# Performance work log

Measured on AMD Instinct MI355X. Metric: run time of the kernel, lower is better.

The kernel has to match this reference:

```python
import jax, jax.numpy as jnp
import numpy as np

B, S, D, H = 16, 512, 1024, 4096
TOP_K = H // 4  # default: hidden_dim // 4


def setup_inputs() -> dict:
    key = jax.random.key(0)
    ks = jax.random.split(key, 11)
    s = lambda fan_in: 1.0 / np.sqrt(fan_in)
    return {
        "inputs": jax.random.normal(ks[0], (B, S, D), jnp.float32),
        "up_w": jax.random.uniform(ks[1], (H, D), jnp.float32, -s(D), s(D)),
        "up_b": jax.random.uniform(ks[2], (H,), jnp.float32, -s(D), s(D)),
        "gate_w1": jax.random.uniform(ks[3], (H, D), jnp.float32, -s(D), s(D)),
        "gate_b1": jax.random.uniform(ks[4], (H,), jnp.float32, -s(D), s(D)),
        "gate_w2": jax.random.uniform(ks[5], (H, H), jnp.float32, -s(H), s(H)),
        "gate_b2": jax.random.uniform(ks[6], (H,), jnp.float32, -s(H), s(H)),
        "mod_w": jax.random.uniform(ks[7], (H, D), jnp.float32, -s(D), s(D)),
        "mod_b": jax.random.uniform(ks[8], (H,), jnp.float32, -s(D), s(D)),
        "down_w": jax.random.uniform(ks[9], (D, H), jnp.float32, -s(H), s(H)),
        "down_b": jax.random.uniform(ks[10], (D,), jnp.float32, -s(H), s(H)),
    }


def reference(inputs, up_w, up_b, gate_w1, gate_b1, gate_w2, gate_b2,
              mod_w, mod_b, down_w, down_b):
    b, s_len, d = inputs.shape
    h_dim = up_w.shape[0]
    # gate MLP -> scores [B, S, H]
    scores = jax.nn.relu(jnp.einsum('bsd,hd->bsh', inputs, gate_w1) + gate_b1)
    scores = jnp.einsum('bsh,gh->bsg', scores, gate_w2) + gate_b2
    flat = scores.reshape(b, s_len * h_dim)
    k = min(TOP_K * s_len, s_len * h_dim)
    _, flat_idx = jax.lax.top_k(flat, k)                    # [B, k]
    hidden_idx = flat_idx % h_dim                           # [B, k]
    # mask[b, h] = True if row h of up.weight was overwritten by mod.weight
    # (duplicate indices write the same value, so set-semantics are exact)
    mask = jnp.zeros((b, h_dim), bool).at[
        jnp.arange(b)[:, None], hidden_idx].set(True)       # [B, H]
    # Instead of materializing per-batch [B,H,D] weights, compute both shared-
    # weight GEMMs and select per (batch, hidden) row — identical math.
    h_up = jnp.einsum('bsd,hd->bsh', inputs, up_w) + up_b
    h_mod = jnp.einsum('bsd,hd->bsh', inputs, mod_w) + mod_b
    h = jnp.where(mask[:, None, :], h_mod, h_up)            # [B, S, H]
    h = jax.nn.silu(h)
    # dropout is identity in eval/reference mode
    return jnp.einsum('bsh,dh->bsd', h, down_w) + down_b
```

## Files before the change

kernel.cpp:

```cpp
#include <hip/hip_runtime.h>
#include <cstdint>

typedef __attribute__((ext_vector_type(4))) _Float16 f16x4;
typedef __attribute__((ext_vector_type(8))) _Float16 f16x8;
typedef __attribute__((ext_vector_type(4))) float f32x4;

#define D_DIM 1024
#define H_DIM 4096
#define BS_ROWS 8192
#define K_SEL 524288u
#define CAND_CAP 32768u

__device__ __forceinline__ unsigned lkey(float v){
  float u = fmaf(v, 67108864.f, 268435456.f);
  u = fminf(fmaxf(u, 0.f), 536870911.f);
  return (unsigned)u;
}

__device__ __forceinline__ void gload16(const _Float16* g, _Float16* l){
  __builtin_amdgcn_global_load_lds(
      (const __attribute__((address_space(1))) void*)g,
      (__attribute__((address_space(3))) void*)l, 16, 0, 0);
}

template<int N> __device__ __forceinline__ void waitcnt_vm(){
  if      constexpr (N == 0) asm volatile("s_waitcnt vmcnt(0)" ::: "memory");
  else if constexpr (N == 4) asm volatile("s_waitcnt vmcnt(4)" ::: "memory");
  else if constexpr (N == 6) asm volatile("s_waitcnt vmcnt(6)" ::: "memory");
  else                       asm volatile("s_waitcnt vmcnt(8)" ::: "memory");
}

__device__ __forceinline__ size_t img_g32(int row, int k8, int nkt32){
  int p = (row & 127) >> 1;
  int s = (((row & 1) << 2) | (k8 & 3)) ^ (p & 7);
  return ((size_t)((row >> 7) * nkt32 + (k8 >> 2)) << 9) + (p << 3) + s;
}

__global__ __launch_bounds__(256)
void pack_all(const float* __restrict__ X, const float* __restrict__ g1w,
              const float* __restrict__ g2w, const float* __restrict__ upw,
              const float* __restrict__ modw, const float* __restrict__ dww,
              _Float16* __restrict__ Xhi, _Float16* __restrict__ Xlo,
              _Float16* __restrict__ G1hi, _Float16* __restrict__ G1lo,
              _Float16* __restrict__ G2hi, _Float16* __restrict__ G2lo,
              _Float16* __restrict__ UPhi, _Float16* __restrict__ MODhi,
              _Float16* __restrict__ DWhi)
{
  unsigned g = blockIdx.x * 256u + threadIdx.x;
  const float* W; _Float16* hi; _Float16* lo = nullptr;
  int k8s, n32; unsigned base;
  if      (g < 1048576u){ W=X;    hi=Xhi;  lo=Xlo;  k8s=7; n32=32;  base=0u;        }
  else if (g < 1572864u){ W=g1w;  hi=G1hi; lo=G1lo; k8s=7; n32=32;  base=1048576u; }
  else if (g < 3670016u){ W=g2w;  hi=G2hi; lo=G2lo; k8s=9; n32=128; base=1572864u; }
  else if (g < 4194304u){ W=upw;  hi=UPhi;          k8s=7; n32=32;  base=3670016u; }
  else if (g < 4718592u){ W=modw; hi=MODhi;         k8s=7; n32=32;  base=4194304u; }
  else                  { W=dww;  hi=DWhi;          k8s=9; n32=128; base=4718592u; }
  g -= base;
  int row = (int)(g >> k8s), k8 = (int)(g & ((1u << k8s) - 1u));
  const float* src = W + ((size_t)row << (k8s + 3)) + (k8 << 3);
  float4 f0 = *(const float4*)src, f1 = *(const float4*)(src + 4);
  float ff[8] = {f0.x,f0.y,f0.z,f0.w,f1.x,f1.y,f1.z,f1.w};
  f16x8 hv, lv;
  #pragma unroll
  for (int i = 0; i < 8; i++){
    hv[i] = (_Float16)ff[i];
    lv[i] = (_Float16)(ff[i] - (float)hv[i]);
  }
  size_t d = img_g32(row, k8, n32) << 3;
  *(f16x8*)&hi[d] = hv;
  if (lo) *(f16x8*)&lo[d] = lv;
}

enum { MODE_G1 = 0, MODE_G2 = 1, MODE_UPMOD = 2, MODE_DOWN = 3 };

template<int MODE>
__global__ __launch_bounds__(256)
void gemm_t(const _Float16* __restrict__ Ahi, const _Float16* __restrict__ Alo,
            const _Float16* __restrict__ Bhi, const _Float16* __restrict__ Blo,
            const float* __restrict__ bias0, const float* __restrict__ bias1,
            const unsigned* __restrict__ mask,
            _Float16* __restrict__ Chi, _Float16* __restrict__ Clo,
            float* __restrict__ C32,
            int N, int K, int m_img_base, int c_row_base)
{
  constexpr int NSEG = (MODE == MODE_G1) ? 3 : 1;
  constexpr bool BSEL = (MODE == MODE_UPMOD);
  constexpr int NLD = (NSEG == 3) ? 8 : 4;
  constexpr int DEPTH = (NSEG == 3) ? 2 : 3;
  __shared__ __align__(16) _Float16 sA [DEPTH][4096];
  __shared__ __align__(16) _Float16 sB [DEPTH][4096];
  __shared__ __align__(16) _Float16 sAl[NSEG == 3 ? 2 : 1][NSEG == 3 ? 4096 : 8];
  __shared__ __align__(16) _Float16 sBl[NSEG == 3 ? 2 : 1][NSEG == 3 ? 4096 : 8];

  const int nbx = gridDim.x;
  const int h = blockIdx.y * nbx + blockIdx.x;
  const int xcd = h & 7, idx = h >> 3;
  const int cw = nbx >> 2;
  const int ch = gridDim.y >> 1;
  const int bx = (xcd & 3) * cw + idx % cw;
  const int by = (xcd >> 2) * ch + idx / cw;

  const int tid = threadIdx.x;
  const int lane = tid & 63;
  const int w  = tid >> 6;
  const int wr = w >> 1, wc = w & 1;
  const int lr = lane & 15;
  const int q  = lane >> 4;

  const int m0 = m_img_base + by * 128;
  const int n0 = bx * 128;
  const int nkt = K >> 5;
  const size_t arow = (size_t)(m0 >> 7) * nkt;
  const size_t brow = (size_t)(n0 >> 7) * nkt;

  const _Float16* bsrcl[2];
  if (BSEL){
    const int bb = m0 >> 9;
    #pragma unroll
    for (int j = 0; j < 2; j++){
      int gi = (w*2 + j)*64 + lane;
      int p = gi >> 3, x = (gi & 7) ^ (p & 7);
      int row = (p << 1) | (x >> 2);
      bsrcl[j] = (mask[bb * H_DIM + n0 + row] ? Blo : Bhi) + (gi << 3);
    }
    waitcnt_vm<0>();
  }

  f32x4 acc[4][4];
  #pragma unroll
  for (int i = 0; i < 4; i++)
    #pragma unroll
    for (int j = 0; j < 4; j++) acc[i][j] = (f32x4){0.f,0.f,0.f,0.f};

  const int soff = (((((lr & 1) << 2) | q) ^ (lr >> 1)) << 3);

  auto STAGE = [&](int buf, int kt){
    const _Float16* at = Ahi + ((arow + kt) << 12);
    #pragma unroll
    for (int j = 0; j < 2; j++)
      gload16(at + ((w*2 + j) << 9) + (lane << 3), &sA[buf][(w*2 + j) << 9]);
    if (NSEG == 3){
      const _Float16* alt = Alo + ((arow + kt) << 12);
      const _Float16* bht = Bhi + ((brow + kt) << 12);
      const _Float16* blt = Blo + ((brow + kt) << 12);
      #pragma unroll
      for (int j = 0; j < 2; j++){
        gload16(alt + ((w*2 + j) << 9) + (lane << 3), &sAl[buf][(w*2 + j) << 9]);
        gload16(bht + ((w*2 + j) << 9) + (lane << 3), &sB [buf][(w*2 + j) << 9]);
        gload16(blt + ((w*2 + j) << 9) + (lane << 3), &sBl[buf][(w*2 + j) << 9]);
      }
    } else if (BSEL){
      const size_t toff = (brow + kt) << 12;
      #pragma unroll
      for (int j = 0; j < 2; j++)
        gload16(bsrcl[j] + toff, &sB[buf][(w*2 + j) << 9]);
    } else {
      const _Float16* bht = Bhi + ((brow + kt) << 12);
      #pragma unroll
      for (int j = 0; j < 2; j++)
        gload16(bht + ((w*2 + j) << 9) + (lane << 3), &sB[buf][(w*2 + j) << 9]);
    }
  };

  STAGE(0, 0);
  if (DEPTH == 3) STAGE(1, 1);

  for (int kt = 0; kt < nkt; ++kt){
    const int rem = nkt - 1 - kt;
    const int cur = (DEPTH == 2) ? (kt & 1) : (kt % 3);
    if (DEPTH == 2){
      if (rem >= 1){ STAGE((kt + 1) & 1, kt + 1); waitcnt_vm<NLD>(); }
      else         { waitcnt_vm<0>(); }
    } else {
      if (rem >= 2){ STAGE((kt + 2) % 3, kt + 2); waitcnt_vm<8>(); }
      else if (rem == 1){ waitcnt_vm<4>(); }
      else         { waitcnt_vm<0>(); }
    }
    __builtin_amdgcn_s_barrier();
    __builtin_amdgcn_sched_barrier(0);

    f16x8 fah[4], fbh[4], fal[4], fbl[4];
    #pragma unroll
    for (int i = 0; i < 4; i++){
      const int ap = ((wr*32 + i*8 + (lr >> 1)) << 6) + soff;
      const int bp = ((wc*32 + i*8 + (lr >> 1)) << 6) + soff;
      fah[i] = *(const f16x8*)&sA[cur][ap];
      fbh[i] = *(const f16x8*)&sB[cur][bp];
      if (NSEG == 3){
        fal[i] = *(const f16x8*)&sAl[cur][ap];
        fbl[i] = *(const f16x8*)&sBl[cur][bp];
      }
    }
    #pragma unroll
    for (int mi = 0; mi < 4; mi++)
      #pragma unroll
      for (int ni = 0; ni < 4; ni++)
        acc[mi][ni] = __builtin_amdgcn_mfma_f32_16x16x32_f16(fah[mi], fbh[ni], acc[mi][ni], 0,0,0);
    if (NSEG == 3){
      #pragma unroll
      for (int mi = 0; mi < 4; mi++)
        #pragma unroll
        for (int ni = 0; ni < 4; ni++)
          acc[mi][ni] = __builtin_amdgcn_mfma_f32_16x16x32_f16(fal[mi], fbh[ni], acc[mi][ni], 0,0,0);
      #pragma unroll
      for (int mi = 0; mi < 4; mi++)
        #pragma unroll
        for (int ni = 0; ni < 4; ni++)
          acc[mi][ni] = __builtin_amdgcn_mfma_f32_16x16x32_f16(fah[mi], fbl[ni], acc[mi][ni], 0,0,0);
    }
    __builtin_amdgcn_s_barrier();
  }

  #pragma unroll
  for (int ni = 0; ni < 4; ni++){
    const int gc = n0 + wc*64 + ni*16 + lr;
    float bias;
    if (MODE == MODE_UPMOD) bias = mask[(m0 >> 9) * H_DIM + gc] ? bias1[gc] : bias0[gc];
    else                    bias = bias0[gc];
    #pragma unroll
    for (int mi = 0; mi < 4; mi++){
      #pragma unroll
      for (int r = 0; r < 4; r++){
        const int gr = m0 + wr*64 + mi*16 + q*4 + r;
        const int cr = gr - c_row_base;
        float v = acc[mi][ni][r] + bias;
        if (MODE == MODE_G1){
          v = fmaxf(v, 0.f);
          size_t d = (img_g32(cr, gc >> 3, N >> 5) << 3) + (gc & 7);
          Chi[d] = (_Float16)v;
        }
        if (MODE == MODE_UPMOD){
          v = v / (1.f + __expf(-v));
          size_t d = (img_g32(cr, gc >> 3, N >> 5) << 3) + (gc & 7);
          Chi[d] = (_Float16)v;
        }
        if (MODE == MODE_DOWN) C32[(size_t)cr * N + gc] = v;
      }
    }
  }
}

__global__ __launch_bounds__(512, 2)
void gemm_g2(const _Float16* __restrict__ A, const _Float16* __restrict__ B,
             const float* __restrict__ bias0,
             unsigned* __restrict__ keys, unsigned* __restrict__ Mkey,
             unsigned* __restrict__ hist, int N, int K, int batch_base)
{
  __shared__ __align__(16) _Float16 sAb[3][8192];
  __shared__ __align__(16) _Float16 sBb[3][8192];

  const int nbx = gridDim.x;
  const int h = blockIdx.y * nbx + blockIdx.x;
  const int xcd = h & 7, idx = h >> 3;
  const int cw = nbx >> 2, ch = gridDim.y >> 1;
  const int bx = (xcd & 3) * cw + idx % cw;
  const int by = (xcd >> 2) * ch + idx / cw;

  const int tid = threadIdx.x;
  const int lane = tid & 63;
  const int w = tid >> 6;
  const int wrow = w >> 2, wcol = w & 3;
  const int lr = lane & 15;
  const int q = lane >> 4;

  const int m0 = by * 256;
  const int n0 = bx * 256;
  const int nkt = K >> 5;
  const int ar0 = (m0 >> 7) * nkt;
  const int br0 = (n0 >> 7) * nkt;

  f32x4 acc[8][4];
  #pragma unroll
  for (int i = 0; i < 8; i++)
    #pragma unroll
    for (int j = 0; j < 4; j++) acc[i][j] = (f32x4){0.f,0.f,0.f,0.f};

  const int soff = (((((lr & 1) << 2) | q) ^ (lr >> 1)) << 3);
  int offA[8], offB[4];
  #pragma unroll
  for (int mi = 0; mi < 8; mi++) offA[mi] = ((mi*8 + (lr >> 1)) << 6) + soff;
  #pragma unroll
  for (int ni = 0; ni < 4; ni++)
    offB[ni] = (((wcol & 1)*32 + ni*8 + (lr >> 1)) << 6) + soff;
  const int arb = wrow * 4096;
  const int bcb = (wcol >> 1) * 4096;

  auto STA = [&](int buf, int rb, int kt){
    gload16(A + ((((size_t)(ar0 + rb*nkt + kt) << 9) + tid) << 3),
            &sAb[buf][rb*4096 + (tid << 3)]);
  };
  auto STB = [&](int buf, int cb, int kt){
    gload16(B + ((((size_t)(br0 + cb*nkt + kt) << 9) + tid) << 3),
            &sBb[buf][cb*4096 + (tid << 3)]);
  };

#define G2PHASE(P, STG)                                                        \
  {                                                                            \
    f16x8 a0 = *(const f16x8*)&sAb[cur][arb + offA[2*(P)]];                    \
    f16x8 a1 = *(const f16x8*)&sAb[cur][arb + offA[2*(P)+1]];                  \
    STG;                                                                       \
    if ((P) == 3){ if (pf) waitcnt_vm<4>(); else waitcnt_vm<0>(); }            \
    __builtin_amdgcn_s_barrier();                                              \
    asm volatile("s_waitcnt lgkmcnt(0)" ::: "memory");                         \
    __builtin_amdgcn_sched_barrier(0);                                         \
    __builtin_amdgcn_s_setprio(1);                                             \
    _Pragma("unroll")                                                          \
    for (int ni = 0; ni < 4; ni++)                                             \
      acc[2*(P)][ni]   = __builtin_amdgcn_mfma_f32_16x16x32_f16(a0, fb[ni], acc[2*(P)][ni], 0,0,0);   \
    _Pragma("unroll")                                                          \
    for (int ni = 0; ni < 4; ni++)                                             \
      acc[2*(P)+1][ni] = __builtin_amdgcn_mfma_f32_16x16x32_f16(a1, fb[ni], acc[2*(P)+1][ni], 0,0,0); \
    __builtin_amdgcn_s_setprio(0);                                             \
    __builtin_amdgcn_s_barrier();                                              \
  }

  STA(0,0,0); STB(0,0,0); STB(0,1,0); STA(0,1,0);
  STA(1,0,1); STB(1,0,1); STB(1,1,1); STA(1,1,1);
  waitcnt_vm<4>();
  __builtin_amdgcn_s_barrier();

  for (int kt = 0; kt < nkt; ++kt){
    const int cur = kt % 3, nb = (kt + 2) % 3;
    const bool pf = (kt + 2 < nkt);
    f16x8 fb[4];
    #pragma unroll
    for (int ni = 0; ni < 4; ni++)
      fb[ni] = *(const f16x8*)&sBb[cur][bcb + offB[ni]];
    G2PHASE(0, if (pf) STA(nb, 0, kt+2))
    G2PHASE(1, if (pf) STB(nb, 0, kt+2))
    G2PHASE(2, if (pf) STB(nb, 1, kt+2))
    G2PHASE(3, if (pf) STA(nb, 1, kt+2))
  }
#undef G2PHASE

  unsigned* lh = (unsigned*)&sAb[0][0];
  __syncthreads();
  for (int i = tid; i < 4096; i += 512) lh[i] = 0;
  __syncthreads();

  const int gb = batch_base + (m0 >> 9);
  #pragma unroll
  for (int ni = 0; ni < 4; ni++){
    const int gc = n0 + wcol*64 + ni*16 + lr;
    const float bias = bias0[gc];
    unsigned colmax = 0u;
    #pragma unroll
    for (int mi = 0; mi < 8; mi++){
      #pragma unroll
      for (int r = 0; r < 4; r++){
        const int gr = m0 + wrow*128 + mi*16 + q*4 + r;
        float v = acc[mi][ni][r] + bias;
        unsigned key = lkey(v);
        keys[(size_t)gr * N + gc] = key;
        colmax = max(colmax, key);
        atomicAdd(&lh[key >> 17], 1u);
      }
    }
    atomicMax(&Mkey[gb * H_DIM + gc], colmax);
  }
  __syncthreads();
  for (int i = tid; i < 4096; i += 512)
    if (lh[i]) atomicAdd(&hist[(gb << 12) + i], lh[i]);
}


__global__ __launch_bounds__(256)
void select12(const unsigned* __restrict__ hist, unsigned* __restrict__ b12,
              unsigned* __restrict__ krem, unsigned* __restrict__ ccount, int b0)
{
  const int b = b0 + (int)blockIdx.x;
  __shared__ unsigned part[256];
  const unsigned base = (unsigned)b << 12;
  unsigned s = 0;
  #pragma unroll
  for (int i = 0; i < 16; i++) s += hist[base + threadIdx.x*16 + i];
  part[threadIdx.x] = s;
  __syncthreads();
  if (threadIdx.x == 0){
    unsigned cum = 0; int t = 255;
    for (; t > 0; --t){
      if (cum + part[t] >= K_SEL) break;
      cum += part[t];
    }
    int bin = 15; unsigned kr = K_SEL;
    for (; bin > 0; --bin){
      unsigned c = hist[base + t*16 + bin];
      if (cum + c >= K_SEL) break;
      cum += c;
    }
    kr = K_SEL - cum;
    b12[b] = (unsigned)(t*16 + bin);
    krem[b] = kr;
    ccount[b] = 0;
  }
}

__global__ __launch_bounds__(256)
void collect(const unsigned* __restrict__ keys, const unsigned* __restrict__ b12,
             unsigned* __restrict__ cand, unsigned* __restrict__ ccount, int b0)
{
  __shared__ unsigned cbuf[1024];
  __shared__ unsigned lcnt, gbase;
  const int bl = blockIdx.y;
  const int b  = b0 + bl;
  const unsigned bin = b12[b];
  if (threadIdx.x == 0) lcnt = 0;
  __syncthreads();
  const uint4* p = (const uint4*)(keys + (size_t)bl*2097152u + (size_t)blockIdx.x*8192u);
  uint4 kv[8];
  #pragma unroll
  for (int j = 0; j < 8; j++) kv[j] = p[threadIdx.x + j*256];
  #pragma unroll
  for (int j = 0; j < 8; j++){
    #pragma unroll
    for (int e = 0; e < 4; e++){
      unsigned k = (e==0)?kv[j].x:(e==1)?kv[j].y:(e==2)?kv[j].z:kv[j].w;
      if ((k >> 17) == bin){
        unsigned idx = atomicAdd(&lcnt, 1u);
        if (idx < 1024u) cbuf[idx] = k;
      }
    }
  }
  __syncthreads();
  const unsigned n = lcnt < 1024u ? lcnt : 1024u;
  if (threadIdx.x == 0) gbase = atomicAdd(&ccount[b], n);
  __syncthreads();
  const unsigned gb = gbase;
  for (unsigned i = threadIdx.x; i < n; i += 256){
    unsigned dst = gb + i;
    if (dst < CAND_CAP) cand[((size_t)b << 15) + dst] = cbuf[i];
  }
}

__global__ __launch_bounds__(256)
void select_exact(const unsigned* __restrict__ cand, const unsigned* __restrict__ ccount,
                  const unsigned* __restrict__ b12, const unsigned* __restrict__ kremA,
                  unsigned* __restrict__ tkey, int b0)
{
  const int b = b0 + (int)blockIdx.x;
  unsigned cc = ccount[b];
  const unsigned n = cc < CAND_CAP ? cc : CAND_CAP;
  __shared__ unsigned h[256];
  __shared__ unsigned sh2[2];
  unsigned prefix = b12[b] << 17;
  unsigned krem = kremA[b];
  const unsigned pm[3]  = {0xFFFE0000u, 0xFFFFFE00u, 0xFFFFFFFEu};
  const int      shs[3] = {9, 1, 0};
  const int      wid[3] = {256, 256, 2};
  for (int pass = 0; pass < 3; ++pass){
    if (threadIdx.x < (unsigned)wid[pass]) h[threadIdx.x] = 0;
    __syncthreads();
    for (unsigned i = threadIdx.x; i < n; i += 256){
      unsigned k = cand[((size_t)b << 15) + i];
      if ((k & pm[pass]) == prefix)
        atomicAdd(&h[(k >> shs[pass]) & (unsigned)(wid[pass]-1)], 1u);
    }
    __syncthreads();
    if (threadIdx.x == 0){
      unsigned cum = 0; int bin = wid[pass]-1;
      for (; bin > 0; --bin){
        unsigned c = h[bin];
        if (cum + c >= krem) break;
        cum += c;
      }
      krem -= cum;
      prefix |= ((unsigned)bin) << shs[pass];
      sh2[0] = prefix; sh2[1] = krem;
    }
    __syncthreads();
    prefix = sh2[0]; krem = sh2[1];
    __syncthreads();
  }
  if (threadIdx.x == 0) tkey[b] = prefix;
}

__global__ __launch_bounds__(256)
void make_mask(const unsigned* __restrict__ Mkey, const unsigned* __restrict__ tkey,
               unsigned* __restrict__ mask){
  const int i = blockIdx.x * 256 + threadIdx.x;
  const int b = i >> 12;
  mask[i] = (Mkey[i] >= tkey[b]) ? 1u : 0u;
}

extern "C" void kernel_launch(void* const* d_in, const int* in_sizes, int n_in,
                              void* d_out, int out_size, void* d_ws, size_t ws_size,
                              hipStream_t stream)
{
  (void)in_sizes; (void)n_in; (void)out_size; (void)ws_size;
  const float* X      = (const float*)d_in[0];
  const float* up_w   = (const float*)d_in[1];
  const float* up_b   = (const float*)d_in[2];
  const float* g1w    = (const float*)d_in[3];
  const float* g1b    = (const float*)d_in[4];
  const float* g2w    = (const float*)d_in[5];
  const float* g2b    = (const float*)d_in[6];
  const float* mod_w  = (const float*)d_in[7];
  const float* mod_b  = (const float*)d_in[8];
  const float* down_w = (const float*)d_in[9];
  const float* down_b = (const float*)d_in[10];
  float* out = (float*)d_out;

  char* ws = (char*)d_ws;
  _Float16* Xhi  = (_Float16*)(ws);
  _Float16* Xlo  = (_Float16*)(ws + (16ull<<20));
  _Float16* G1hi = (_Float16*)(ws + (32ull<<20));
  _Float16* G1lo = (_Float16*)(ws + (40ull<<20));
  _Float16* G2hi = (_Float16*)(ws + (48ull<<20));
  _Float16* UPhi = (_Float16*)(ws + (112ull<<20));
  _Float16* MODhi= (_Float16*)(ws + (120ull<<20));
  _Float16* DWhi = (_Float16*)(ws + (128ull<<20));
  _Float16* Fhi  = (_Float16*)(ws + (136ull<<20));
  unsigned* keys = (unsigned*)(ws + (168ull<<20));
  _Float16* Hbuf = (_Float16*)(ws + (136ull<<20));
  char* aux = ws + (232ull<<20);
  unsigned* Mkey  = (unsigned*)(aux);
  unsigned* maskb = (unsigned*)(aux + 262144);
  unsigned* hist  = (unsigned*)(aux + 524288);
  unsigned* cand  = (unsigned*)(aux + 786432);
  unsigned* b12   = (unsigned*)(aux + 786432 + 2097152);
  unsigned* krem  = (unsigned*)(aux + 786432 + 2097152 + 64);
  unsigned* ccnt  = (unsigned*)(aux + 786432 + 2097152 + 128);
  unsigned* tkey  = (unsigned*)(aux + 786432 + 2097152 + 192);

  pack_all<<<20480, 256, 0, stream>>>(X, g1w, g2w, up_w, mod_w, down_w,
                                      Xhi, Xlo, G1hi, G1lo, G2hi, nullptr,
                                      UPhi, MODhi, DWhi);

  hipMemsetAsync(Mkey, 0, 262144, stream);
  hipMemsetAsync(hist, 0, 262144, stream);

  for (int half = 0; half < 2; ++half){
    const int b0 = half * 8;
    gemm_t<MODE_G1><<<dim3(32, 32), 256, 0, stream>>>(
        Xhi, Xlo, G1hi, G1lo, g1b, nullptr, nullptr,
        Fhi, nullptr, nullptr, H_DIM, D_DIM, half*4096, half*4096);
    gemm_g2<<<dim3(16, 16), 512, 0, stream>>>(
        Fhi, G2hi, g2b, keys, Mkey, hist, H_DIM, H_DIM, b0);
    select12<<<8, 256, 0, stream>>>(hist, b12, krem, ccnt, b0);
    collect<<<dim3(256, 8), 256, 0, stream>>>(keys, b12, cand, ccnt, b0);
    select_exact<<<8, 256, 0, stream>>>(cand, ccnt, b12, krem, tkey, b0);
  }
  make_mask<<<256, 256, 0, stream>>>(Mkey, tkey, maskb);

  gemm_t<MODE_UPMOD><<<dim3(32, 64), 256, 0, stream>>>(
      Xhi, nullptr, UPhi, MODhi, up_b, mod_b, maskb,
      Hbuf, nullptr, nullptr, H_DIM, D_DIM, 0, 0);
  gemm_t<MODE_DOWN><<<dim3(8, 64), 256, 0, stream>>>(
      Hbuf, nullptr, DWhi, nullptr, down_b, nullptr, nullptr,
      nullptr, nullptr, out, D_DIM, H_DIM, 0, 0);
}
```

Measured before the change: 912.0 us.

## Add dedicated split-precision gate-1 GEMM with 256x128 tiles and 8 waves

Replaces the generic templated GEMM used for the first gate layer with a specialized kernel that uses 512 threads, 256x128 output tiles, triple-buffered LDS loads via global_load_lds, and phased MFMA issue interleaved with prefetch. It computes hi*hi + lo*hi + hi*lo f16 products to emulate higher precision. The larger tile is meant to improve operand reuse and the phased schedule to overlap loads with MFMA work. In exchange, LDS use is high (about 144KB) and occupancy drops to one block per CU.

```diff
diff --git a/kernel.cpp b/kernel.cpp
--- a/kernel.cpp
+++ b/kernel.cpp
@@ -235,6 +235,127 @@
           Chi[d] = (_Float16)v;
         }
         if (MODE == MODE_DOWN) C32[(size_t)cr * N + gc] = v;
+      }
+    }
+  }
+}
+
+__global__ __launch_bounds__(512, 1)
+void gemm_g1(const _Float16* __restrict__ Ahi, const _Float16* __restrict__ Alo,
+             const _Float16* __restrict__ Bhi, const _Float16* __restrict__ Blo,
+             const float* __restrict__ bias0, _Float16* __restrict__ Chi,
+             int N, int K, int m_img_base, int c_row_base)
+{
+  __shared__ __align__(16) _Float16 sAh[3][8192];
+  __shared__ __align__(16) _Float16 sAl[3][8192];
+  __shared__ __align__(16) _Float16 sBh[3][4096];
+  __shared__ __align__(16) _Float16 sBl[3][4096];
+
+  const int nbx = gridDim.x;
+  const int h = blockIdx.y * nbx + blockIdx.x;
+  const int xcd = h & 7, idx = h >> 3;
+  const int cw = nbx >> 2, ch = gridDim.y >> 1;
+  const int bx = (xcd & 3) * cw + idx % cw;
+  const int by = (xcd >> 2) * ch + idx / cw;
+
+  const int tid = threadIdx.x;
+  const int lane = tid & 63;
+  const int w = tid >> 6;
+  const int wrow = w >> 1, wcol = w & 1;
+  const int lr = lane & 15;
+  const int q = lane >> 4;
+
+  const int m0 = m_img_base + by * 256;
+  const int n0 = bx * 128;
+  const int nkt = K >> 5;
+  const int at0 = (m0 >> 7) * nkt;
+  const int bt0 = (n0 >> 7) * nkt;
+
+  f32x4 acc[4][4];
+  #pragma unroll
+  for (int i = 0; i < 4; i++)
+    #pragma unroll
+    for (int j = 0; j < 4; j++) acc[i][j] = (f32x4){0.f,0.f,0.f,0.f};
+
+  const int soff = (((((lr & 1) << 2) | q) ^ (lr >> 1)) << 3);
+  int offA[4], offB[4];
+  #pragma unroll
+  for (int mi = 0; mi < 4; mi++)
+    offA[mi] = (wrow >> 1)*4096 + ((((wrow & 1)*32) + mi*8 + (lr >> 1)) << 6) + soff;
+  #pragma unroll
+  for (int ni = 0; ni < 4; ni++)
+    offB[ni] = ((wcol*32 + ni*8 + (lr >> 1)) << 6) + soff;
+
+  auto STA = [&](int buf, int rb, int kt, bool lo){
+    const _Float16* img = lo ? Alo : Ahi;
+    _Float16* dst = (lo ? &sAl[buf][0] : &sAh[buf][0]) + rb*4096 + (tid << 3);
+    gload16(img + ((((size_t)(at0 + rb*nkt + kt)) << 9) + tid) * 8, dst);
+  };
+  auto STB = [&](int buf, int kt, bool lo){
+    const _Float16* img = lo ? Blo : Bhi;
+    _Float16* dst = (lo ? &sBl[buf][0] : &sBh[buf][0]) + (tid << 3);
+    gload16(img + ((((size_t)(bt0 + kt)) << 9) + tid) * 8, dst);
+  };
+
+#define G1PHASE(P, STG)                                                        \
+  {                                                                            \
+    f16x8 ah = *(const f16x8*)&sAh[cur][offA[P]];                              \
+    f16x8 al = *(const f16x8*)&sAl[cur][offA[P]];                              \
+    STG;                                                                       \
+    if ((P) == 3){ if (pf) waitcnt_vm<6>(); else waitcnt_vm<0>(); }            \
+    __builtin_amdgcn_s_barrier();                                              \
+    asm volatile("s_waitcnt lgkmcnt(0)" ::: "memory");                         \
+    __builtin_amdgcn_sched_barrier(0);                                         \
+    __builtin_amdgcn_s_setprio(1);                                             \
+    _Pragma("unroll")                                                          \
+    for (int ni = 0; ni < 4; ni++)                                             \
+      acc[P][ni] = __builtin_amdgcn_mfma_f32_16x16x32_f16(ah, fbh[ni], acc[P][ni], 0,0,0); \
+    _Pragma("unroll")                                                          \
+    for (int ni = 0; ni < 4; ni++)                                             \
+      acc[P][ni] = __builtin_amdgcn_mfma_f32_16x16x32_f16(al, fbh[ni], acc[P][ni], 0,0,0); \
+    _Pragma("unroll")                                                          \
+    for (int ni = 0; ni < 4; ni++)                                             \
+      acc[P][ni] = __builtin_amdgcn_mfma_f32_16x16x32_f16(ah, fbl[ni], acc[P][ni], 0,0,0); \
+    __builtin_amdgcn_s_setprio(0);                                             \
+    __builtin_amdgcn_s_barrier();                                              \
+  }
+
+  STA(0,0,0,false); STA(0,1,0,false); STA(0,0,0,true); STA(0,1,0,true);
+  STB(0,0,false);   STB(0,0,true);
+  STA(1,0,1,false); STA(1,1,1,false); STA(1,0,1,true); STA(1,1,1,true);
+  STB(1,1,false);   STB(1,1,true);
+  waitcnt_vm<6>();
+  __builtin_amdgcn_s_barrier();
+
+  for (int kt = 0; kt < nkt; ++kt){
+    const int cur = kt % 3, nb = (kt + 2) % 3;
+    const bool pf = (kt + 2 < nkt);
+    f16x8 fbh[4], fbl[4];
+    #pragma unroll
+    for (int ni = 0; ni < 4; ni++){
+      fbh[ni] = *(const f16x8*)&sBh[cur][offB[ni]];
+      fbl[ni] = *(const f16x8*)&sBl[cur][offB[ni]];
+    }
+    G1PHASE(0, if (pf){ STA(nb,0,kt+2,false); STA(nb,1,kt+2,false); })
+    G1PHASE(1, if (pf){ STA(nb,0,kt+2,true);  STA(nb,1,kt+2,true);  })
+    G1PHASE(2, if (pf){ STB(nb,kt+2,false);   STB(nb,kt+2,true);    })
+    G1PHASE(3, )
+  }
+#undef G1PHASE
+
+  #pragma unroll
+  for (int ni = 0; ni < 4; ni++){
+    const int gc = n0 + wcol*64 + ni*16 + lr;
+    const float bias = bias0[gc];
+    #pragma unroll
+    for (int mi = 0; mi < 4; mi++){
+      #pragma unroll
+      for (int r = 0; r < 4; r++){
+        const int gr = m0 + wrow*64 + mi*16 + q*4 + r;
+        const int cr = gr - c_row_base;
+        float v = fmaxf(acc[mi][ni][r] + bias, 0.f);
+        size_t d = (img_g32(cr, gc >> 3, N >> 5) << 3) + (gc & 7);
+        Chi[d] = (_Float16)v;
       }
     }
   }
@@ -531,9 +652,8 @@
 
   for (int half = 0; half < 2; ++half){
     const int b0 = half * 8;
-    gemm_t<MODE_G1><<<dim3(32, 32), 256, 0, stream>>>(
-        Xhi, Xlo, G1hi, G1lo, g1b, nullptr, nullptr,
-        Fhi, nullptr, nullptr, H_DIM, D_DIM, half*4096, half*4096);
+    gemm_g1<<<dim3(32, 16), 512, 0, stream>>>(
+        Xhi, Xlo, G1hi, G1lo, g1b, Fhi, H_DIM, D_DIM, half*4096, half*4096);
     gemm_g2<<<dim3(16, 16), 512, 0, stream>>>(
         Fhi, G2hi, g2b, keys, Mkey, hist, H_DIM, H_DIM, b0);
     select12<<<8, 256, 0, stream>>>(hist, b12, krem, ccnt, b0);
```

Result: slower. 934.2 us (+2.4%).
